# Kernel tuning notes

Hardware: AMD Instinct MI355X
Metric: run time of the kernel (lower is better)

The kernel has to match this reference:

```python
import jax, jax.numpy as jnp
import numpy as np

B, T, D = 4, 2048, 512
H, DK = 4, 16
MU = 1.0


def _xavier(key, shape):
    lim = float(np.sqrt(6.0 / (shape[0] + shape[1])))
    return jax.random.uniform(key, shape, jnp.float32, -lim, lim)


def setup_inputs() -> dict:
    key = jax.random.key(0)
    ks = jax.random.split(key, 9)
    x = jax.random.normal(ks[0], (B, T, D), jnp.float32)
    Wq = _xavier(ks[1], (D, H * DK))
    Wk = _xavier(ks[2], (D, H * DK))
    Wv = _xavier(ks[3], (D, H * DK))
    # W_a is zero-initialized in the module; use small random values so the
    # decay path is exercised non-trivially.
    Wa = 0.02 * jax.random.normal(ks[4], (D, H), jnp.float32)
    ba = 0.02 * jax.random.normal(ks[5], (H,), jnp.float32)
    Wg = 0.02 * jax.random.normal(ks[6], (D, H * DK), jnp.float32)
    bg = jnp.zeros((H * DK,), jnp.float32)
    Wo = _xavier(ks[7], (H * DK, D))
    return {"x": x, "Wq": Wq, "Wk": Wk, "Wv": Wv, "Wa": Wa, "ba": ba,
            "Wg": Wg, "bg": bg, "Wo": Wo}


def reference(x, Wq, Wk, Wv, Wa, ba, Wg, bg, Wo):
    b_, t_, _ = x.shape
    q = (x @ Wq).reshape(b_, t_, H, DK)
    k = (x @ Wk).reshape(b_, t_, H, DK)
    v = (x @ Wv).reshape(b_, t_, H, DK)
    # bid b_s = <q_s, k_s>/sqrt(dk); decay a_s = -softplus(x W_a + c_a) <= 0
    bid = jnp.sum(q * k, axis=-1) / np.sqrt(DK)      # (B, T, H)
    a = -jax.nn.softplus(x @ Wa + ba)                # (B, T, H)
    # Closed form of the sequential scan:
    #   scores[t, s] = bid[s] + sum_{r=s+1..t} a[r] = (bid[s] - cumA[s]) + cumA[t]
    # Row-constant cumA[t] cancels in the softmax, so the attention weights are
    # a causal softmax over mu * (bid[s] - cumA[s]).
    cumA = jnp.cumsum(a, axis=1)                     # (B, T, H)
    lg = (bid - cumA).transpose(0, 2, 1)             # (B, H, S_keys)
    mask = jnp.tril(jnp.ones((t_, t_), bool))        # keys s <= query t
    scores = jnp.where(mask[None, None], MU * lg[:, :, None, :], -jnp.inf)
    w = jax.nn.softmax(scores, axis=-1)              # (B, H, T, S)
    y = jnp.einsum('bhts,bshd->bthd', w, v)          # (B, T, H, DK)
    gate = jax.nn.sigmoid(x @ Wg + bg).reshape(b_, t_, H, DK)
    y = (y * gate).reshape(b_, t_, H * DK)
    return y @ Wo
```

## Files before the change

### kernel.cpp

```cpp
#include <hip/hip_runtime.h>
#include <math.h>

#define B_    4
#define T_    2048
#define D_    512
#define H_    4
#define ROWS_ 8192
#define CHSZ_ 128
#define NCHK_ 16

typedef unsigned short ushort_t;
typedef unsigned int   uint_t;
typedef __attribute__((ext_vector_type(8))) __bf16         bfx8;
typedef __attribute__((ext_vector_type(8))) unsigned short u16x8;
typedef __attribute__((ext_vector_type(4))) float          fx4;

__device__ __forceinline__ ushort_t f2bf(float f) {
    union { float f; uint_t u; } v; v.f = f;
    return (ushort_t)((v.u + 0x7FFFu + ((v.u >> 16) & 1u)) >> 16);
}
__device__ __forceinline__ float bf2f(ushort_t u) {
    union { uint_t u; float f; } v; v.u = ((uint_t)u) << 16; return v.f;
}

__global__ __launch_bounds__(256) void gemm_scanA(const float* __restrict__ x,
                                                  const float* __restrict__ Wa,
                                                  const float* __restrict__ ba,
                                                  const float* __restrict__ Wq,
                                                  const float* __restrict__ Wk,
                                                  const float* __restrict__ Wv,
                                                  const float* __restrict__ Wg,
                                                  float* __restrict__ stateWS,
                                                  float* __restrict__ chunkSum,
                                                  ushort_t* __restrict__ gBuf) {
    __shared__ ushort_t As[128 * 72];
    __shared__ ushort_t Bs[64 * 72];
    __shared__ float s_a[128];
    __shared__ float s_a0;
    __shared__ float s_wmax[2];
    __shared__ float s_tot[17];

    const int rc = blockIdx.x & 63;
    const int h  = blockIdx.x >> 6;
    const int m0 = rc * 128;
    const int b  = rc >> 4, chunk = rc & 15;
    const int bh = b * 4 + h;

    const int tid = threadIdx.x;
    const int wave = tid >> 6, lane = tid & 63;
    const int fr = lane & 15, quad = lane >> 4;
    const int sr = tid >> 3, sc = (tid & 7) * 8;

    const int colw = h * 16 + (sr & 15);
    const float* W1 = (sr < 16) ? Wq : Wk;
    const float* W2 = (sr < 16) ? Wv : Wg;

    fx4 acc[2][4];
    #pragma unroll
    for (int i = 0; i < 2; i++)
        #pragma unroll
        for (int j = 0; j < 4; j++) acc[i][j] = (fx4)0.f;

    float pa[4] = {0.f, 0.f, 0.f, 0.f};

    float4 raF[4][2];
    float  rbF[2][8];
    float  rwa[8];
    #pragma unroll
    for (int s = 0; s < 4; s++) {
        const float* xp = x + (size_t)(m0 + s * 32 + sr) * D_ + sc;
        raF[s][0] = *(const float4*)xp;
        raF[s][1] = *(const float4*)(xp + 4);
    }
    #pragma unroll
    for (int j = 0; j < 8; j++) {
        rbF[0][j] = W1[(size_t)(sc + j) * 64 + colw];
        rbF[1][j] = W2[(size_t)(sc + j) * 64 + colw];
        rwa[j]    = Wa[(size_t)(sc + j) * 4 + h];
    }

    for (int it = 0; it < 8; it++) {
        #pragma unroll
        for (int s = 0; s < 4; s++) {
            float xv[8] = {raF[s][0].x, raF[s][0].y, raF[s][0].z, raF[s][0].w,
                           raF[s][1].x, raF[s][1].y, raF[s][1].z, raF[s][1].w};
            u16x8 u;
            #pragma unroll
            for (int j = 0; j < 8; j++) {
                u[j] = f2bf(xv[j]);
                pa[s] = fmaf(xv[j], rwa[j], pa[s]);
            }
            *(u16x8*)&As[(s * 32 + sr) * 72 + sc] = u;
        }
        #pragma unroll
        for (int s = 0; s < 2; s++) {
            u16x8 u;
            #pragma unroll
            for (int j = 0; j < 8; j++) u[j] = f2bf(rbF[s][j]);
            *(u16x8*)&Bs[(s * 32 + sr) * 72 + sc] = u;
        }
        __syncthreads();
        if (it < 7) {
            const int k0 = (it + 1) * 64;
            #pragma unroll
            for (int s = 0; s < 4; s++) {
                const float* xp = x + (size_t)(m0 + s * 32 + sr) * D_ + k0 + sc;
                raF[s][0] = *(const float4*)xp;
                raF[s][1] = *(const float4*)(xp + 4);
            }
            #pragma unroll
            for (int j = 0; j < 8; j++) {
                rbF[0][j] = W1[(size_t)(k0 + sc + j) * 64 + colw];
                rbF[1][j] = W2[(size_t)(k0 + sc + j) * 64 + colw];
                rwa[j]    = Wa[(size_t)(k0 + sc + j) * 4 + h];
            }
        }
        #pragma unroll
        for (int ks = 0; ks < 64; ks += 32) {
            bfx8 af[2], bfr[4];
            #pragma unroll
            for (int mi = 0; mi < 2; mi++)
                af[mi] = *(const bfx8*)&As[(wave * 32 + mi * 16 + fr) * 72 + ks + quad * 8];
            #pragma unroll
            for (int ni = 0; ni < 4; ni++)
                bfr[ni] = *(const bfx8*)&Bs[(ni * 16 + fr) * 72 + ks + quad * 8];
            #pragma unroll
            for (int mi = 0; mi < 2; mi++)
                #pragma unroll
                for (int ni = 0; ni < 4; ni++)
                    acc[mi][ni] = __builtin_amdgcn_mfma_f32_16x16x32_bf16(af[mi], bfr[ni], acc[mi][ni], 0, 0, 0);
        }
        __syncthreads();
    }

    #pragma unroll
    for (int mi = 0; mi < 2; mi++)
        #pragma unroll
        for (int ni = 0; ni < 4; ni++)
            #pragma unroll
            for (int r = 0; r < 4; r++) {
                int rl = wave * 32 + mi * 16 + quad * 4 + r;
                int cl = ni * 16 + fr;
                As[rl * 72 + cl] = f2bf(acc[mi][ni][r]);
            }

    #pragma unroll
    for (int s = 0; s < 4; s++) {
        #pragma unroll
        for (int m = 1; m < 8; m <<= 1) pa[s] += __shfl_xor(pa[s], m, 8);
    }
    if ((tid & 7) == 0) {
        const float bah = ba[h];
        #pragma unroll
        for (int s = 0; s < 4; s++) {
            float z = pa[s] + bah;
            s_a[s * 32 + sr] = -(fmaxf(z, 0.f) + log1pf(expf(-fabsf(z))));
        }
    }
    __syncthreads();

    const bool active = (tid < 128);
    float bid = 0.f, a = 0.f;
    float v[16];
    if (active) {
        const ushort_t* ct = &As[tid * 72];
        u16x8 q0 = *(const u16x8*)(ct +  0), q1 = *(const u16x8*)(ct +  8);
        u16x8 k0 = *(const u16x8*)(ct + 16), k1 = *(const u16x8*)(ct + 24);
        u16x8 v0 = *(const u16x8*)(ct + 32), v1 = *(const u16x8*)(ct + 40);
        #pragma unroll
        for (int j = 0; j < 8; j++) {
            bid = fmaf(bf2f(q0[j]), bf2f(k0[j]), bid);
            bid = fmaf(bf2f(q1[j]), bf2f(k1[j]), bid);
            v[j]     = bf2f(v0[j]);
            v[8 + j] = bf2f(v1[j]);
        }
        bid *= 0.25f;
        a = s_a[tid];
    }

    float ca = a;
    #pragma unroll
    for (int off = 1; off < 64; off <<= 1) {
        float up = __shfl_up(ca, off);
        if (lane >= off) ca += up;
    }
    if (tid == 63) s_a0 = ca;
    __syncthreads();
    if (active && wave == 1) ca += s_a0;

    float lg = bid - ca;

    float Mw = active ? lg : -1e30f;
    #pragma unroll
    for (int off = 32; off; off >>= 1) Mw = fmaxf(Mw, __shfl_xor(Mw, off));
    if (active && lane == 0) s_wmax[wave] = Mw;
    __syncthreads();
    const float M0 = s_wmax[0], M1 = s_wmax[1];
    const float Mc = fmaxf(M0, M1);

    float d = active ? __expf(lg - Mw) : 0.f;
    float n[16];
    #pragma unroll
    for (int j = 0; j < 16; j++) n[j] = d * v[j];
    #pragma unroll
    for (int off = 1; off < 64; off <<= 1) {
        float ud = __shfl_up(d, off);
        float un[16];
        #pragma unroll
        for (int j = 0; j < 16; j++) un[j] = __shfl_up(n[j], off);
        if (lane >= off) {
            d += ud;
            #pragma unroll
            for (int j = 0; j < 16; j++) n[j] += un[j];
        }
    }
    if (tid == 63) {
        s_tot[0] = d;
        #pragma unroll
        for (int j = 0; j < 16; j++) s_tot[1 + j] = n[j];
    }
    __syncthreads();
    if (active && wave == 1) {
        float al = __expf(M0 - Mc), be = __expf(M1 - Mc);
        d = s_tot[0] * al + d * be;
        #pragma unroll
        for (int j = 0; j < 16; j++) n[j] = s_tot[1 + j] * al + n[j] * be;
    }
    const float myM = (wave == 0) ? M0 : Mc;

    if (active) {
        const int t = chunk * CHSZ_ + tid;
        const size_t eidx = (size_t)bh * T_ + t;
        stateWS[eidx] = myM;
        stateWS[32768 + eidx] = d;
        #pragma unroll
        for (int j = 0; j < 16; j++) stateWS[(size_t)(2 + j) * 32768 + eidx] = n[j];

        const ushort_t* ct = &As[tid * 72];
        u16x8 g0 = *(const u16x8*)(ct + 48), g1 = *(const u16x8*)(ct + 56);
        *(u16x8*)(gBuf + eidx * 16)     = g0;
        *(u16x8*)(gBuf + eidx * 16 + 8) = g1;

        if (tid == 127) {
            float* cs = chunkSum + (size_t)(bh * NCHK_ + chunk) * 20;
            cs[0] = Mc; cs[1] = d;
            #pragma unroll
            for (int j = 0; j < 16; j++) cs[2 + j] = n[j];
            cs[18] = ca;
        }
    }
}

__global__ __launch_bounds__(256) void scan_gemm(const float* __restrict__ stateWS,
                                                 const float* __restrict__ chunkSum,
                                                 const ushort_t* __restrict__ gBuf,
                                                 const float* __restrict__ bg,
                                                 const float* __restrict__ Wo,
                                                 float* __restrict__ C) {
    __shared__ ushort_t Ys[64 * 72];
    __shared__ ushort_t Bs[128 * 72];
    __shared__ float s_pref[4][18];

    const int m0 = blockIdx.y * 64;
    const int n0 = blockIdx.x * 128;
    const int b  = m0 >> 11;
    const int tt = m0 & 2047;
    const int chunk = tt >> 7;

    const int tid = threadIdx.x;
    const int wave = tid >> 6, lane = tid & 63;

    const int sr = tid >> 3, sc = (tid & 7) * 8;
    #pragma unroll
    for (int s = 0; s < 4; s++) {
        int rr = s * 32 + sr;
        u16x8 u;
        #pragma unroll
        for (int j = 0; j < 8; j++)
            u[j] = f2bf(Wo[(size_t)(sc + j) * D_ + n0 + rr]);
        *(u16x8*)&Bs[rr * 72 + sc] = u;
    }

    const int h = wave, r = lane;
    const int bh = b * 4 + h;
    const size_t eidx = (size_t)bh * T_ + tt + r;
    float m_row = stateWS[eidx];
    float d_row = stateWS[32768 + eidx];
    float n_row[16];
    #pragma unroll
    for (int j = 0; j < 16; j++) n_row[j] = stateWS[(size_t)(2 + j) * 32768 + eidx];
    u16x8 g0 = *(const u16x8*)(gBuf + eidx * 16);
    u16x8 g1 = *(const u16x8*)(gBuf + eidx * 16 + 8);

    if (wave == 0) {
        const int hh = lane >> 4, p = lane & 15;
        const int bhh = b * 4 + hh;
        float mf = -1e30f, dd = 0.f, aT = 0.f;
        float nn[16];
        #pragma unroll
        for (int j = 0; j < 16; j++) nn[j] = 0.f;
        if (p < chunk) {
            const float* cs = chunkSum + (size_t)(bhh * NCHK_ + p) * 20;
            mf = cs[0]; dd = cs[1];
            #pragma unroll
            for (int j = 0; j < 16; j++) nn[j] = cs[2 + j];
            aT = cs[18];
        }
        float off = aT;
        #pragma unroll
        for (int s = 1; s < 16; s <<= 1) {
            float t2 = __shfl_down(off, s, 16);
            if (p + s < chunk) off += t2;
        }
        if (p < chunk) mf += off;
        #pragma unroll
        for (int s = 1; s < 16; s <<= 1) {
            float m2 = __shfl_xor(mf, s, 16);
            float d2 = __shfl_xor(dd, s, 16);
            float mx = fmaxf(mf, m2);
            float al = __expf(mf - mx), be = __expf(m2 - mx);
            #pragma unroll
            for (int j = 0; j < 16; j++) {
                float n2 = __shfl_xor(nn[j], s, 16);
                nn[j] = nn[j] * al + n2 * be;
            }
            dd = dd * al + d2 * be;
            mf = mx;
        }
        if (p == 0) {
            s_pref[hh][0] = mf; s_pref[hh][1] = dd;
            #pragma unroll
            for (int j = 0; j < 16; j++) s_pref[hh][2 + j] = nn[j];
        }
    }
    __syncthreads();

    {
        const float M = s_pref[h][0], D = s_pref[h][1];
        const float mx = fmaxf(M, m_row);
        const float al = __expf(M - mx), be = __expf(m_row - mx);
        const float invd = 1.f / (D * al + d_row * be);
        u16x8 o0, o1;
        #pragma unroll
        for (int j = 0; j < 16; j++) {
            float Nj = s_pref[h][2 + j] * al + n_row[j] * be;
            float gpre = ((j < 8) ? bf2f(g0[j]) : bf2f(g1[j - 8])) + bg[h * 16 + j];
            float gate = 1.f / (1.f + __expf(-gpre));
            ushort_t yb = f2bf(Nj * invd * gate);
            if (j < 8) o0[j] = yb; else o1[j - 8] = yb;
        }
        *(u16x8*)&Ys[r * 72 + h * 16]     = o0;
        *(u16x8*)&Ys[r * 72 + h * 16 + 8] = o1;
    }
    __syncthreads();

    const int wr = wave >> 1, wc = wave & 1;
    const int fr = lane & 15, quad = lane >> 4;
    fx4 acc[2][4];
    #pragma unroll
    for (int i = 0; i < 2; i++)
        #pragma unroll
        for (int j = 0; j < 4; j++) acc[i][j] = (fx4)0.f;

    #pragma unroll
    for (int ks = 0; ks < 64; ks += 32) {
        bfx8 af[2], bfr[4];
        #pragma unroll
        for (int mi = 0; mi < 2; mi++)
            af[mi] = *(const bfx8*)&Ys[(wr * 32 + mi * 16 + fr) * 72 + ks + quad * 8];
        #pragma unroll
        for (int ni = 0; ni < 4; ni++)
            bfr[ni] = *(const bfx8*)&Bs[(wc * 64 + ni * 16 + fr) * 72 + ks + quad * 8];
        #pragma unroll
        for (int mi = 0; mi < 2; mi++)
            #pragma unroll
            for (int ni = 0; ni < 4; ni++)
                acc[mi][ni] = __builtin_amdgcn_mfma_f32_16x16x32_bf16(af[mi], bfr[ni], acc[mi][ni], 0, 0, 0);
    }

    #pragma unroll
    for (int mi = 0; mi < 2; mi++)
        #pragma unroll
        for (int ni = 0; ni < 4; ni++)
            #pragma unroll
            for (int rr = 0; rr < 4; rr++) {
                int orow = m0 + wr * 32 + mi * 16 + quad * 4 + rr;
                int ocol = n0 + wc * 64 + ni * 16 + fr;
                C[(size_t)orow * D_ + ocol] = acc[mi][ni][rr];
            }
}

extern "C" void kernel_launch(void* const* d_in, const int* in_sizes, int n_in,
                              void* d_out, int out_size, void* d_ws, size_t ws_size,
                              hipStream_t stream) {
    const float* x  = (const float*)d_in[0];
    const float* Wq = (const float*)d_in[1];
    const float* Wk = (const float*)d_in[2];
    const float* Wv = (const float*)d_in[3];
    const float* Wa = (const float*)d_in[4];
    const float* ba = (const float*)d_in[5];
    const float* Wg = (const float*)d_in[6];
    const float* bg = (const float*)d_in[7];
    const float* Wo = (const float*)d_in[8];
    float* out = (float*)d_out;

    char* w = (char*)d_ws;
    float*    stateWS  = (float*)w;     w += (size_t)18 * 32768 * 4;
    float*    chunkSum = (float*)w;     w += 256 * 20 * 4;
    ushort_t* gBuf     = (ushort_t*)w;  w += (size_t)32768 * 16 * 2;

    gemm_scanA<<<256, 256, 0, stream>>>(x, Wa, ba, Wq, Wk, Wv, Wg,
                                        stateWS, chunkSum, gBuf);
    scan_gemm<<<dim3(4, 128), 256, 0, stream>>>(stateWS, chunkSum, gBuf, bg, Wo, out);
}
```

Measured before the change: 114.4 us.

## Prepack weights into transposed bf16 buffers with a separate pre-kernel

Adds a pack_w kernel that converts Wq/Wk/Wv/Wg into one concatenated, transposed bf16 matrix and Wo into a transposed bf16 matrix. The two main kernels then load weights with vectorized 16-byte reads instead of strided scalar fp32 loads followed by per-element bf16 conversion. The Wa column is also staged once into shared memory rather than reloaded every k-step. The cost is an extra kernel launch plus a workspace write and read of the packed weights on every call.

```diff
diff --git a/kernel.cpp b/kernel.cpp
--- a/kernel.cpp
+++ b/kernel.cpp
@@ -23,18 +23,37 @@
     union { uint_t u; float f; } v; v.u = ((uint_t)u) << 16; return v.f;
 }
 
+__global__ __launch_bounds__(256) void pack_w(const float* __restrict__ Wq,
+                                              const float* __restrict__ Wk,
+                                              const float* __restrict__ Wv,
+                                              const float* __restrict__ Wg,
+                                              const float* __restrict__ Wo,
+                                              ushort_t* __restrict__ WcatT2,
+                                              ushort_t* __restrict__ WoT) {
+    int idx = blockIdx.x * 256 + threadIdx.x;
+    if (idx < 256 * 512) {
+        int n = idx >> 9, d = idx & 511;
+        int h = n >> 6, r = n & 63, part = r >> 4, j = r & 15;
+        int col = h * 16 + j;
+        const float* W = (part == 0) ? Wq : (part == 1) ? Wk : (part == 2) ? Wv : Wg;
+        WcatT2[idx] = f2bf(W[(size_t)d * 64 + col]);
+    } else {
+        int r = idx - 256 * 512;
+        int n = r >> 6, k = r & 63;
+        WoT[r] = f2bf(Wo[(size_t)k * 512 + n]);
+    }
+}
+
 __global__ __launch_bounds__(256) void gemm_scanA(const float* __restrict__ x,
                                                   const float* __restrict__ Wa,
                                                   const float* __restrict__ ba,
-                                                  const float* __restrict__ Wq,
-                                                  const float* __restrict__ Wk,
-                                                  const float* __restrict__ Wv,
-                                                  const float* __restrict__ Wg,
+                                                  const ushort_t* __restrict__ WcatT2,
                                                   float* __restrict__ stateWS,
                                                   float* __restrict__ chunkSum,
                                                   ushort_t* __restrict__ gBuf) {
     __shared__ ushort_t As[128 * 72];
     __shared__ ushort_t Bs[64 * 72];
+    __shared__ float s_wa[512];
     __shared__ float s_a[128];
     __shared__ float s_a0;
     __shared__ float s_wmax[2];
@@ -43,6 +62,7 @@
     const int rc = blockIdx.x & 63;
     const int h  = blockIdx.x >> 6;
     const int m0 = rc * 128;
+    const int n0 = h * 64;
     const int b  = rc >> 4, chunk = rc & 15;
     const int bh = b * 4 + h;
 
@@ -51,9 +71,8 @@
     const int fr = lane & 15, quad = lane >> 4;
     const int sr = tid >> 3, sc = (tid & 7) * 8;
 
-    const int colw = h * 16 + (sr & 15);
-    const float* W1 = (sr < 16) ? Wq : Wk;
-    const float* W2 = (sr < 16) ? Wv : Wg;
+    s_wa[tid * 2]     = Wa[(size_t)(tid * 2) * 4 + h];
+    s_wa[tid * 2 + 1] = Wa[(size_t)(tid * 2 + 1) * 4 + h];
 
     fx4 acc[2][4];
     #pragma unroll
@@ -64,8 +83,7 @@
     float pa[4] = {0.f, 0.f, 0.f, 0.f};
 
     float4 raF[4][2];
-    float  rbF[2][8];
-    float  rwa[8];
+    u16x8  rb[2];
     #pragma unroll
     for (int s = 0; s < 4; s++) {
         const float* xp = x + (size_t)(m0 + s * 32 + sr) * D_ + sc;
@@ -73,13 +91,13 @@
         raF[s][1] = *(const float4*)(xp + 4);
     }
     #pragma unroll
-    for (int j = 0; j < 8; j++) {
-        rbF[0][j] = W1[(size_t)(sc + j) * 64 + colw];
-        rbF[1][j] = W2[(size_t)(sc + j) * 64 + colw];
-        rwa[j]    = Wa[(size_t)(sc + j) * 4 + h];
-    }
+    for (int s = 0; s < 2; s++)
+        rb[s] = *(const u16x8*)(WcatT2 + (size_t)(n0 + s * 32 + sr) * D_ + sc);
+
+    __syncthreads();
 
     for (int it = 0; it < 8; it++) {
+        const int kb = it * 64 + sc;
         #pragma unroll
         for (int s = 0; s < 4; s++) {
             float xv[8] = {raF[s][0].x, raF[s][0].y, raF[s][0].z, raF[s][0].w,
@@ -88,17 +106,13 @@
             #pragma unroll
             for (int j = 0; j < 8; j++) {
                 u[j] = f2bf(xv[j]);
-                pa[s] = fmaf(xv[j], rwa[j], pa[s]);
+                pa[s] = fmaf(xv[j], s_wa[kb + j], pa[s]);
             }
             *(u16x8*)&As[(s * 32 + sr) * 72 + sc] = u;
         }
         #pragma unroll
-        for (int s = 0; s < 2; s++) {
-            u16x8 u;
-            #pragma unroll
-            for (int j = 0; j < 8; j++) u[j] = f2bf(rbF[s][j]);
-            *(u16x8*)&Bs[(s * 32 + sr) * 72 + sc] = u;
-        }
+        for (int s = 0; s < 2; s++)
+            *(u16x8*)&Bs[(s * 32 + sr) * 72 + sc] = rb[s];
         __syncthreads();
         if (it < 7) {
             const int k0 = (it + 1) * 64;
@@ -109,11 +123,8 @@
                 raF[s][1] = *(const float4*)(xp + 4);
             }
             #pragma unroll
-            for (int j = 0; j < 8; j++) {
-                rbF[0][j] = W1[(size_t)(k0 + sc + j) * 64 + colw];
-                rbF[1][j] = W2[(size_t)(k0 + sc + j) * 64 + colw];
-                rwa[j]    = Wa[(size_t)(k0 + sc + j) * 4 + h];
-            }
+            for (int s = 0; s < 2; s++)
+                rb[s] = *(const u16x8*)(WcatT2 + (size_t)(n0 + s * 32 + sr) * D_ + k0 + sc);
         }
         #pragma unroll
         for (int ks = 0; ks < 64; ks += 32) {
@@ -255,7 +266,7 @@
                                                  const float* __restrict__ chunkSum,
                                                  const ushort_t* __restrict__ gBuf,
                                                  const float* __restrict__ bg,
-                                                 const float* __restrict__ Wo,
+                                                 const ushort_t* __restrict__ WoT,
                                                  float* __restrict__ C) {
     __shared__ ushort_t Ys[64 * 72];
     __shared__ ushort_t Bs[128 * 72];
@@ -274,11 +285,7 @@
     #pragma unroll
     for (int s = 0; s < 4; s++) {
         int rr = s * 32 + sr;
-        u16x8 u;
-        #pragma unroll
-        for (int j = 0; j < 8; j++)
-            u[j] = f2bf(Wo[(size_t)(sc + j) * D_ + n0 + rr]);
-        *(u16x8*)&Bs[rr * 72 + sc] = u;
+        *(u16x8*)&Bs[rr * 72 + sc] = *(const u16x8*)(WoT + (size_t)(n0 + rr) * 64 + sc);
     }
 
     const int h = wave, r = lane;
@@ -405,11 +412,14 @@
     float* out = (float*)d_out;
 
     char* w = (char*)d_ws;
+    ushort_t* WcatT2   = (ushort_t*)w;  w += 256 * 512 * 2;
+    ushort_t* WoT      = (ushort_t*)w;  w += 512 * 64 * 2;
     float*    stateWS  = (float*)w;     w += (size_t)18 * 32768 * 4;
     float*    chunkSum = (float*)w;     w += 256 * 20 * 4;
     ushort_t* gBuf     = (ushort_t*)w;  w += (size_t)32768 * 16 * 2;
 
-    gemm_scanA<<<256, 256, 0, stream>>>(x, Wa, ba, Wq, Wk, Wv, Wg,
+    pack_w<<<640, 256, 0, stream>>>(Wq, Wk, Wv, Wg, Wo, WcatT2, WoT);
+    gemm_scanA<<<256, 256, 0, stream>>>(x, Wa, ba, WcatT2,
                                         stateWS, chunkSum, gBuf);
-    scan_gemm<<<dim3(4, 128), 256, 0, stream>>>(stateWS, chunkSum, gBuf, bg, Wo, out);
-}
+    scan_gemm<<<dim3(4, 128), 256, 0, stream>>>(stateWS, chunkSum, gBuf, bg, WoT, out);
+}
```

Result: faster. 103.6 us (-9.5%).
